# Optimization experiments

Measured on AMD Instinct MI355X. Metric: run time of the kernel, lower is better.

Reference implementation:

```python
import jax, jax.numpy as jnp
import numpy as np

N, D, H, E, K = 4096, 1024, 2048, 8, 2


def setup_inputs() -> dict:
    key = jax.random.key(0)
    ks = jax.random.split(key, 4)
    x = jax.random.normal(ks[0], (N, D), dtype=jnp.float32)
    w_gate = jax.random.normal(ks[1], (D, E), dtype=jnp.float32) * 0.02
    w1 = jax.random.normal(ks[2], (E, D, H), dtype=jnp.float32) * (1.0 / np.sqrt(D))
    b1 = jnp.zeros((E, H), dtype=jnp.float32)
    w2 = jax.random.normal(ks[3], (E, H, D), dtype=jnp.float32) * (1.0 / np.sqrt(H))
    b2 = jnp.zeros((E, D), dtype=jnp.float32)
    return {"x": x, "w_gate": w_gate, "w1": w1, "b1": b1, "w2": w2, "b2": b2}


def reference(x, w_gate, w1, b1, w2, b2):
    # --- top-k gating ---
    logits = x @ w_gate                      # [N, E]
    top_vals, top_idx = jax.lax.top_k(logits, K)   # [N, K]
    gates_k = jax.nn.softmax(top_vals, axis=-1)    # softmax over selected experts
    # scatter sparse gates into dense [N, E] combine weights (zeros off top-k)
    gates = jnp.zeros((x.shape[0], E), dtype=x.dtype)
    gates = gates.at[jnp.arange(x.shape[0])[:, None], top_idx].set(gates_k)
    # --- expert FFNs (computed densely over experts, combined sparsely) ---
    h = jax.nn.gelu(jnp.einsum('nd,edh->neh', x, w1) + b1[None])   # [N, E, H]
    y = jnp.einsum('neh,ehd->ned', h, w2) + b2[None]               # [N, E, D]
    out = jnp.einsum('ne,ned->nd', gates, y)                        # [N, D]
    return out
```

## Files before the change

kernel.cpp:

```cpp
#include <hip/hip_runtime.h>
#include <math.h>
#include <stdint.h>

#define N_TOK 4096
#define DIM   1024
#define HID   2048
#define NE    8
#define NROWS (N_TOK * 2)
#define LDST  72
#define OBST  128
#define TPT   16
#define CAP1  144
#define CAP2  72

typedef __attribute__((ext_vector_type(8))) short bf16x8;
typedef __attribute__((ext_vector_type(4))) float f32x4;

__device__ __forceinline__ unsigned short f2bf(float f) {
    union { unsigned int i; float f; } v; v.f = f;
    unsigned int u = v.i;
    return (unsigned short)((u + 0x7FFFu + ((u >> 16) & 1u)) >> 16);
}
__device__ __forceinline__ int clampi(int v, int lo, int hi) {
    return v < lo ? lo : (v > hi ? hi : v);
}
__device__ __forceinline__ void cvt8(const float* p, unsigned short* o) {
    float4 a = *(const float4*)p;
    float4 b = *(const float4*)(p + 4);
    o[0] = f2bf(a.x); o[1] = f2bf(a.y); o[2] = f2bf(a.z); o[3] = f2bf(a.w);
    o[4] = f2bf(b.x); o[5] = f2bf(b.y); o[6] = f2bf(b.z); o[7] = f2bf(b.w);
}
__device__ __forceinline__ float fast_gelu(float v) {
    float c = 0.7978845608028654f * (v + 0.044715f * v * v * v);
    float t = 1.f - 2.f / (1.f + __expf(2.f * c));
    return 0.5f * v * (1.f + t);
}
__device__ __forceinline__ void gload_lds16(const void* g, void* l) {
    __builtin_amdgcn_global_load_lds(
        (const __attribute__((address_space(1))) unsigned int*)g,
        (__attribute__((address_space(3))) unsigned int*)l,
        16, 0, 0);
}

__global__ __launch_bounds__(256) void gate_kernel(
    const float* __restrict__ x, const float* __restrict__ wg,
    unsigned short* __restrict__ top_e, float* __restrict__ top_g)
{
    int wave = threadIdx.x >> 6;
    int lane = threadIdx.x & 63;
    int n = blockIdx.x * 4 + wave;
    if (n >= N_TOK) return;
    float acc[NE];
#pragma unroll
    for (int e = 0; e < NE; e++) acc[e] = 0.f;
    const float* xrow = x + (size_t)n * DIM;
    for (int d = lane; d < DIM; d += 64) {
        float xv = xrow[d];
        float4 wa = *(const float4*)(wg + (size_t)d * NE);
        float4 wb = *(const float4*)(wg + (size_t)d * NE + 4);
        acc[0] += xv * wa.x; acc[1] += xv * wa.y;
        acc[2] += xv * wa.z; acc[3] += xv * wa.w;
        acc[4] += xv * wb.x; acc[5] += xv * wb.y;
        acc[6] += xv * wb.z; acc[7] += xv * wb.w;
    }
#pragma unroll
    for (int e = 0; e < NE; e++) {
        float v = acc[e];
#pragma unroll
        for (int off = 32; off > 0; off >>= 1) v += __shfl_xor(v, off, 64);
        acc[e] = v;
    }
    if (lane == 0) {
        int e0 = 0; float v0 = acc[0];
#pragma unroll
        for (int e = 1; e < NE; e++) if (acc[e] > v0) { v0 = acc[e]; e0 = e; }
        int e1 = (e0 == 0) ? 1 : 0; float v1 = acc[e1];
#pragma unroll
        for (int e = 0; e < NE; e++) if (e != e0 && acc[e] > v1) { v1 = acc[e]; e1 = e; }
        float s = expf(v1 - v0);
        float g0 = 1.f / (1.f + s);
        float g1 = s / (1.f + s);
        top_e[n] = (unsigned short)(e0 | (e1 << 8));
        top_g[2 * n + 0] = g0;
        top_g[2 * n + 1] = g1;
    }
}

__global__ __launch_bounds__(256) void scatter_plan_kernel(
    const unsigned short* __restrict__ top_e, const float* __restrict__ top_g,
    int* __restrict__ row_tok, float* __restrict__ row_gate,
    int* __restrict__ work1, int* __restrict__ work2)
{
    __shared__ int lpre[256][NE];
    __shared__ int etot[NE], ebase[NE];
    __shared__ int Tst[NE + 1];
    __shared__ int kept1[NE], ovb1[NE], fb1[NE + 1];
    __shared__ int kept2[NE], ovb2[NE], fb2[NE + 1];
    int t = threadIdx.x;

    unsigned long long c64 = 0ull;
    unsigned short te[TPT];
#pragma unroll
    for (int i = 0; i < TPT; i++) {
        int v = top_e[t * TPT + i];
        te[i] = (unsigned short)v;
        c64 += 1ull << ((v & 7) * 8);
        c64 += 1ull << (((v >> 8) & 7) * 8);
    }
#pragma unroll
    for (int e = 0; e < NE; e++) lpre[t][e] = (int)((c64 >> (e * 8)) & 0xFF);
    __syncthreads();

    if (t < NE) {
        int s = 0;
        for (int i = 0; i < 256; i++) { int c = lpre[i][t]; lpre[i][t] = s; s += c; }
        etot[t] = s;
    }
    __syncthreads();
    if (t == 0) {
        int b = 0, ts = 0;
#pragma unroll
        for (int e = 0; e < NE; e++) {
            ebase[e] = b; b += etot[e];
            Tst[e] = ts; ts += (etot[e] + 127) >> 7;
        }
        Tst[NE] = ts;
        int ob = 0, fs = 0;
#pragma unroll
        for (int e = 0; e < NE; e++) {
            int it = 16 * ((etot[e] + 127) >> 7);
            kept1[e] = (it < CAP1) ? it : CAP1;
            ovb1[e] = ob; ob += it - kept1[e];
            fb1[e] = fs; fs += CAP1 - kept1[e];
        }
        fb1[NE] = fs;
        ob = 0; fs = 0;
#pragma unroll
        for (int e = 0; e < NE; e++) {
            int it = 8 * ((etot[e] + 127) >> 7);
            kept2[e] = (it < CAP2) ? it : CAP2;
            ovb2[e] = ob; ob += it - kept2[e];
            fb2[e] = fs; fs += CAP2 - kept2[e];
        }
        fb2[NE] = fs;
    }
    __syncthreads();

    for (int i = t; i < NE * CAP1; i += 256) work1[i] = -1;
    for (int i = t; i < NE * CAP2; i += 256) work2[i] = -1;
    __syncthreads();

    int S = Tst[NE];
    for (int idx = t; idx < S * 16; idx += 256) {
        int s = idx >> 4, j = idx & 15;
        int e = 0;
#pragma unroll
        for (int k = 1; k < NE; k++) if (s >= Tst[k]) e = k;
        int sl = s - Tst[e];
        int gr0 = ebase[e] + sl * 128;
        int nv = etot[e] - sl * 128; if (nv > 128) nv = 128;
        int item = (gr0 << 16) | (nv << 8) | (e << 4) | j;
        int q = sl * 16 + j;
        int pos;
        if (q < kept1[e]) pos = e * CAP1 + q;
        else {
            int o = ovb1[e] + (q - kept1[e]);
            int xc = 0;
#pragma unroll
            for (int k = 1; k < NE; k++) if (o >= fb1[k]) xc = k;
            pos = xc * CAP1 + kept1[xc] + (o - fb1[xc]);
        }
        work1[clampi(pos, 0, NE * CAP1 - 1)] = item;
    }
    for (int idx = t; idx < S * 8; idx += 256) {
        int s = idx >> 3, j = idx & 7;
        int e = 0;
#pragma unroll
        for (int k = 1; k < NE; k++) if (s >= Tst[k]) e = k;
        int sl = s - Tst[e];
        int gr0 = ebase[e] + sl * 128;
        int nv = etot[e] - sl * 128; if (nv > 128) nv = 128;
        int item = (gr0 << 16) | (nv << 8) | (e << 4) | j;
        int q = sl * 8 + j;
        int pos;
        if (q < kept2[e]) pos = e * CAP2 + q;
        else {
            int o = ovb2[e] + (q - kept2[e]);
            int xc = 0;
#pragma unroll
            for (int k = 1; k < NE; k++) if (o >= fb2[k]) xc = k;
            pos = xc * CAP2 + kept2[xc] + (o - fb2[xc]);
        }
        work2[clampi(pos, 0, NE * CAP2 - 1)] = item;
    }

#pragma unroll
    for (int i = 0; i < TPT; i++) {
        int n = t * TPT + i;
        int v = te[i];
#pragma unroll
        for (int k = 0; k < 2; k++) {
            int e = (k ? (v >> 8) : v) & 7;
            int r = clampi(ebase[e] + lpre[t][e]++, 0, NROWS - 1);
            row_tok[r]  = (n << 1) | k;
            row_gate[r] = top_g[2 * n + k];
        }
    }
}

__global__ __launch_bounds__(256) void pack_x_kernel(
    const float* __restrict__ x, unsigned short* __restrict__ xb)
{
    size_t i = (size_t)(blockIdx.x * 256 + threadIdx.x) * 8;
    unsigned short o[8];
    cvt8(x + i, o);
    *(uint4*)(xb + i) = *(uint4*)o;
}

__global__ __launch_bounds__(256) void transpose_kernel(
    const float* __restrict__ in, unsigned short* __restrict__ outp, int K, int N)
{
    int e  = blockIdx.z;
    int kb = blockIdx.x;
    int nb = blockIdx.y;
    __shared__ __align__(16) unsigned short tile[64 * LDST];
    int t = threadIdx.x;

    int r = t >> 2, cq = t & 3;
    const float* sp = in + ((size_t)e * K + kb * 64 + r) * N + nb * 64 + cq * 16;
    unsigned short v[16];
    cvt8(sp, v);
    cvt8(sp + 8, v + 8);
    *(uint4*)(&tile[r * LDST + cq * 16 + 0]) = *(uint4*)(v + 0);
    *(uint4*)(&tile[r * LDST + cq * 16 + 8]) = *(uint4*)(v + 8);
    __syncthreads();

    int c = t >> 2, kq = t & 3;
    unsigned short o[16];
#pragma unroll
    for (int i = 0; i < 16; i++) o[i] = tile[(kq * 16 + i) * LDST + c];
    unsigned short* dp = outp + ((size_t)e * N + nb * 64 + c) * K + kb * 64 + kq * 16;
    *(uint4*)(dp + 0) = *(uint4*)(o + 0);
    *(uint4*)(dp + 8) = *(uint4*)(o + 8);
}

__global__ __launch_bounds__(256) void ffn1_fast6(
    const unsigned short* __restrict__ xb,
    const unsigned short* __restrict__ w1t,
    const float* __restrict__ b1,
    const int* __restrict__ work1,
    const int* __restrict__ row_tok,
    unsigned short* __restrict__ h)
{
    int lid = blockIdx.x;
    int wv = work1[(lid & 7) * CAP1 + (lid >> 3)];
    if (wv < 0) return;
    int nb     = wv & 15;
    int e      = (wv >> 4) & 7;
    int nvalid = (wv >> 8) & 0xFF;
    int gr0    = ((unsigned)wv) >> 16;

    __shared__ __align__(16) unsigned short lds[2 * 8192];
    __shared__ int ltok[128];

    int t = threadIdx.x;
    if (t < 128) {
        int rl = clampi(t, 0, nvalid - 1);
        int idx = clampi(gr0 + rl, 0, NROWS - 1);
        ltok[t] = clampi(row_tok[idx] >> 1, 0, N_TOK - 1);
    }
    __syncthreads();

    const int n0 = nb * 128;
    int w = t >> 6;
    const unsigned short* ga[4];
    const unsigned short* gb[4];
    int lofs[4];
#pragma unroll
    for (int i = 0; i < 4; i++) {
        int idx = i * 256 + t;
        int row = idx >> 3, cc = idx & 7;
        int ccs = cc ^ (row & 7);
        ga[i] = xb + (size_t)ltok[row] * DIM + ccs * 8;
        gb[i] = w1t + ((size_t)e * HID + n0 + row) * DIM + ccs * 8;
        lofs[i] = i * 2048 + w * 512;
    }

    int lane = t & 63, quad = lane >> 4, ln = lane & 15;
    int wr = w >> 1, wc = w & 1;
    int xr = ln & 7;
    f32x4 acc[4][4];
#pragma unroll
    for (int i = 0; i < 4; i++)
#pragma unroll
        for (int j = 0; j < 4; j++) acc[i][j] = (f32x4){0.f, 0.f, 0.f, 0.f};

    for (int kt = 0; kt < DIM / 64; kt++) {
        int k0 = kt * 64;
#pragma unroll
        for (int i = 0; i < 4; i++) {
            gload_lds16(ga[i] + k0, lds + lofs[i]);
            gload_lds16(gb[i] + k0, lds + 8192 + lofs[i]);
        }
        __syncthreads();
#pragma unroll
        for (int kk = 0; kk < 2; kk++) {
            bf16x8 af[4], bf[4];
#pragma unroll
            for (int s = 0; s < 4; s++)
                af[s] = *(const bf16x8*)(&lds[(wr * 64 + s * 16 + ln) * 64 + (((kk * 4 + quad) ^ xr) * 8)]);
#pragma unroll
            for (int s = 0; s < 4; s++)
                bf[s] = *(const bf16x8*)(&lds[8192 + (wc * 64 + s * 16 + ln) * 64 + (((kk * 4 + quad) ^ xr) * 8)]);
#pragma unroll
            for (int i = 0; i < 4; i++)
#pragma unroll
                for (int j = 0; j < 4; j++)
                    acc[i][j] = __builtin_amdgcn_mfma_f32_16x16x32_bf16(af[i], bf[j], acc[i][j], 0, 0, 0);
        }
        __syncthreads();
    }

    unsigned short* ob = lds;
#pragma unroll
    for (int j = 0; j < 4; j++) {
        int colL = wc * 64 + j * 16 + ln;
        float bias = b1[e * HID + n0 + colL];
#pragma unroll
        for (int i = 0; i < 4; i++) {
#pragma unroll
            for (int r = 0; r < 4; r++) {
                int m = wr * 64 + i * 16 + quad * 4 + r;
                ob[m * OBST + colL] = f2bf(fast_gelu(acc[i][j][r] + bias));
            }
        }
    }
    __syncthreads();
#pragma unroll
    for (int it = 0; it < 8; it++) {
        int idx = it * 256 + t;
        int m = idx >> 4, ch = idx & 15;
        if (m < nvalid)
            *(uint4*)(h + (size_t)(gr0 + m) * HID + n0 + ch * 8) = *(const uint4*)(ob + m * OBST + ch * 8);
    }
}

__global__ __launch_bounds__(256) void ffn2_fast8(
    const unsigned short* __restrict__ h,
    const unsigned short* __restrict__ w2t,
    const float* __restrict__ b2,
    const int* __restrict__ work2,
    const int* __restrict__ row_tok,
    const float* __restrict__ row_gate,
    float* __restrict__ out,
    float* __restrict__ ybuf1)
{
    int lid = blockIdx.x;
    int wv = work2[(lid & 7) * CAP2 + (lid >> 3)];
    if (wv < 0) return;
    int nb     = wv & 15;
    int e      = (wv >> 4) & 7;
    int nvalid = (wv >> 8) & 0xFF;
    int gr0    = ((unsigned)wv) >> 16;

    __shared__ __align__(16) unsigned short lds[2 * 8192];
    __shared__ int   ltok2[128];
    __shared__ float lgate[128];

    int t = threadIdx.x;
    if (t < 128) {
        int rl = clampi(t, 0, nvalid - 1);
        int idx = clampi(gr0 + rl, 0, NROWS - 1);
        ltok2[t] = clampi(row_tok[idx], 0, 2 * N_TOK - 1);
        lgate[t] = row_gate[idx];
    }
    __syncthreads();

    const int n0 = nb * 128;
    int w = t >> 6;
    const unsigned short* ga[4];
    const unsigned short* gb[4];
    int lofs[4];
#pragma unroll
    for (int i = 0; i < 4; i++) {
        int idx = i * 256 + t;
        int row = idx >> 3, cc = idx & 7;
        int ccs = cc ^ (row & 7);
        int arow = clampi(gr0 + row, 0, NROWS - 1);
        ga[i] = h + (size_t)arow * HID + ccs * 8;
        gb[i] = w2t + ((size_t)e * DIM + n0 + row) * HID + ccs * 8;
        lofs[i] = i * 2048 + w * 512;
    }

    int lane = t & 63, quad = lane >> 4, ln = lane & 15;
    int wr = w >> 1, wc = w & 1;
    int xr = ln & 7;
    f32x4 acc[4][4];
#pragma unroll
    for (int i = 0; i < 4; i++)
#pragma unroll
        for (int j = 0; j < 4; j++) acc[i][j] = (f32x4){0.f, 0.f, 0.f, 0.f};

    for (int kt = 0; kt < HID / 64; kt++) {
        int k0 = kt * 64;
#pragma unroll
        for (int i = 0; i < 4; i++) {
            gload_lds16(ga[i] + k0, lds + lofs[i]);
            gload_lds16(gb[i] + k0, lds + 8192 + lofs[i]);
        }
        __syncthreads();
#pragma unroll
        for (int kk = 0; kk < 2; kk++) {
            bf16x8 af[4], bf[4];
#pragma unroll
            for (int s = 0; s < 4; s++)
                af[s] = *(const bf16x8*)(&lds[(wr * 64 + s * 16 + ln) * 64 + (((kk * 4 + quad) ^ xr) * 8)]);
#pragma unroll
            for (int s = 0; s < 4; s++)
                bf[s] = *(const bf16x8*)(&lds[8192 + (wc * 64 + s * 16 + ln) * 64 + (((kk * 4 + quad) ^ xr) * 8)]);
#pragma unroll
            for (int i = 0; i < 4; i++)
#pragma unroll
                for (int j = 0; j < 4; j++)
                    acc[i][j] = __builtin_amdgcn_mfma_f32_16x16x32_bf16(af[i], bf[j], acc[i][j], 0, 0, 0);
        }
        __syncthreads();
    }

#pragma unroll
    for (int j = 0; j < 4; j++) {
        int col = n0 + wc * 64 + j * 16 + ln;
        float bias = b2[e * DIM + col];
#pragma unroll
        for (int i = 0; i < 4; i++) {
#pragma unroll
            for (int r = 0; r < 4; r++) {
                int m = wr * 64 + i * 16 + quad * 4 + r;
                if (m < nvalid) {
                    int rt  = ltok2[m];
                    int tok = rt >> 1;
                    float vv = (acc[i][j][r] + bias) * lgate[m];
                    float* dst = (rt & 1) ? ybuf1 : out;
                    dst[(size_t)tok * DIM + col] = vv;
                }
            }
        }
    }
}

__global__ __launch_bounds__(256) void combine_kernel(
    float4* __restrict__ out4, const float4* __restrict__ y4)
{
    int i = blockIdx.x * 256 + threadIdx.x;
    float4 a = out4[i];
    float4 b = y4[i];
    out4[i] = make_float4(a.x + b.x, a.y + b.y, a.z + b.z, a.w + b.w);
}

__global__ __launch_bounds__(256) void zero_out_kernel(float* __restrict__ out) {
    int i = blockIdx.x * 256 + threadIdx.x;
    out[i] = 0.f;
}

extern "C" void kernel_launch(void* const* d_in, const int* in_sizes, int n_in,
                              void* d_out, int out_size, void* d_ws, size_t ws_size,
                              hipStream_t stream) {
    const float* x  = (const float*)d_in[0];
    const float* wg = (const float*)d_in[1];
    const float* w1 = (const float*)d_in[2];
    const float* b1 = (const float*)d_in[3];
    const float* w2 = (const float*)d_in[4];
    const float* b2 = (const float*)d_in[5];
    float* out = (float*)d_out;

    char* ws = (char*)d_ws;
    unsigned short* top_e    = (unsigned short*)(ws + 256);
    float*          top_g    = (float*)(ws + 8448);
    int*            row_tok  = (int*)(ws + 41216);
    float*          row_gate = (float*)(ws + 73984);
    int*            work1    = (int*)(ws + 106752);
    int*            work2    = (int*)(ws + 111360);

    const size_t WT_OFF    = (size_t)1 << 17;
    const size_t HBUF_OFF  = WT_OFF + (size_t)NE * DIM * HID * 2;
    const size_t YBUF_OFF  = HBUF_OFF + (size_t)NROWS * HID * 2;
    const size_t NEEDED    = YBUF_OFF + (size_t)N_TOK * DIM * 4;

    if (ws_size < NEEDED) {
        zero_out_kernel<<<dim3(N_TOK * DIM / 256), dim3(256), 0, stream>>>(out);
        return;
    }

    unsigned short* wt    = (unsigned short*)(ws + WT_OFF);
    unsigned short* hbuf  = (unsigned short*)(ws + HBUF_OFF);
    float*          ybuf1 = (float*)(ws + YBUF_OFF);
    unsigned short* xb    = (unsigned short*)(ws + YBUF_OFF);

    gate_kernel<<<dim3(N_TOK / 4), dim3(256), 0, stream>>>(x, wg, top_e, top_g);
    scatter_plan_kernel<<<dim3(1), dim3(256), 0, stream>>>(top_e, top_g, row_tok, row_gate, work1, work2);
    pack_x_kernel<<<dim3(N_TOK * DIM / (256 * 8)), dim3(256), 0, stream>>>(x, xb);
    transpose_kernel<<<dim3(DIM / 64, HID / 64, NE), dim3(256), 0, stream>>>(w1, wt, DIM, HID);
    ffn1_fast6<<<dim3(NE * CAP1), dim3(256), 0, stream>>>(xb, wt, b1, work1, row_tok, hbuf);
    transpose_kernel<<<dim3(HID / 64, DIM / 64, NE), dim3(256), 0, stream>>>(w2, wt, HID, DIM);
    ffn2_fast8<<<dim3(NE * CAP2), dim3(256), 0, stream>>>(hbuf, wt, b2, work2, row_tok, row_gate, out, ybuf1);
    combine_kernel<<<dim3(N_TOK * DIM / 1024), dim3(256), 0, stream>>>((float4*)out, (const float4*)ybuf1);
}
```

Baseline: 374.7 us.

## Split FFN2 reduction dimension in two with atomic accumulation, reusing FFN1 work plan

The second expert GEMM now splits its hidden (K) dimension into two halves, doubling the number of work items so it reuses the ffn1 work list (16 items per 128-row slab). Partial results are accumulated with atomicAdd into out and ybuf1, which are zeroed by two new kernels beforehand; bias is added only by the first half. This aims to improve occupancy and load balance across CUs for the FFN2 phase, at the cost of atomic traffic, two extra zeroing passes and nondeterministic summation order.

New measurement: 420.2 us. 1.12x slower.

```diff
diff --git a/kernel.cpp b/kernel.cpp
--- a/kernel.cpp
+++ b/kernel.cpp
@@ -11,7 +11,6 @@
 #define OBST  128
 #define TPT   16
 #define CAP1  144
-#define CAP2  72
 
 typedef __attribute__((ext_vector_type(8))) short bf16x8;
 typedef __attribute__((ext_vector_type(4))) float f32x4;
@@ -89,13 +88,12 @@
 __global__ __launch_bounds__(256) void scatter_plan_kernel(
     const unsigned short* __restrict__ top_e, const float* __restrict__ top_g,
     int* __restrict__ row_tok, float* __restrict__ row_gate,
-    int* __restrict__ work1, int* __restrict__ work2)
+    int* __restrict__ work1)
 {
     __shared__ int lpre[256][NE];
     __shared__ int etot[NE], ebase[NE];
     __shared__ int Tst[NE + 1];
     __shared__ int kept1[NE], ovb1[NE], fb1[NE + 1];
-    __shared__ int kept2[NE], ovb2[NE], fb2[NE + 1];
     int t = threadIdx.x;
 
     unsigned long long c64 = 0ull;
@@ -134,20 +132,10 @@
             fb1[e] = fs; fs += CAP1 - kept1[e];
         }
         fb1[NE] = fs;
-        ob = 0; fs = 0;
-#pragma unroll
-        for (int e = 0; e < NE; e++) {
-            int it = 8 * ((etot[e] + 127) >> 7);
-            kept2[e] = (it < CAP2) ? it : CAP2;
-            ovb2[e] = ob; ob += it - kept2[e];
-            fb2[e] = fs; fs += CAP2 - kept2[e];
-        }
-        fb2[NE] = fs;
     }
     __syncthreads();
 
     for (int i = t; i < NE * CAP1; i += 256) work1[i] = -1;
-    for (int i = t; i < NE * CAP2; i += 256) work2[i] = -1;
     __syncthreads();
 
     int S = Tst[NE];
@@ -172,27 +160,6 @@
         }
         work1[clampi(pos, 0, NE * CAP1 - 1)] = item;
     }
-    for (int idx = t; idx < S * 8; idx += 256) {
-        int s = idx >> 3, j = idx & 7;
-        int e = 0;
-#pragma unroll
-        for (int k = 1; k < NE; k++) if (s >= Tst[k]) e = k;
-        int sl = s - Tst[e];
-        int gr0 = ebase[e] + sl * 128;
-        int nv = etot[e] - sl * 128; if (nv > 128) nv = 128;
-        int item = (gr0 << 16) | (nv << 8) | (e << 4) | j;
-        int q = sl * 8 + j;
-        int pos;
-        if (q < kept2[e]) pos = e * CAP2 + q;
-        else {
-            int o = ovb2[e] + (q - kept2[e]);
-            int xc = 0;
-#pragma unroll
-            for (int k = 1; k < NE; k++) if (o >= fb2[k]) xc = k;
-            pos = xc * CAP2 + kept2[xc] + (o - fb2[xc]);
-        }
-        work2[clampi(pos, 0, NE * CAP2 - 1)] = item;
-    }
 
 #pragma unroll
     for (int i = 0; i < TPT; i++) {
@@ -345,20 +312,22 @@
     }
 }
 
-__global__ __launch_bounds__(256) void ffn2_fast8(
+__global__ __launch_bounds__(256) void ffn2_fast9(
     const unsigned short* __restrict__ h,
     const unsigned short* __restrict__ w2t,
     const float* __restrict__ b2,
-    const int* __restrict__ work2,
+    const int* __restrict__ work1,
     const int* __restrict__ row_tok,
     const float* __restrict__ row_gate,
     float* __restrict__ out,
     float* __restrict__ ybuf1)
 {
     int lid = blockIdx.x;
-    int wv = work2[(lid & 7) * CAP2 + (lid >> 3)];
+    int wv = work1[(lid & 7) * CAP1 + (lid >> 3)];
     if (wv < 0) return;
-    int nb     = wv & 15;
+    int j4     = wv & 15;
+    int nb     = j4 & 7;
+    int kh     = j4 >> 3;
     int e      = (wv >> 4) & 7;
     int nvalid = (wv >> 8) & 0xFF;
     int gr0    = ((unsigned)wv) >> 16;
@@ -377,6 +346,7 @@
     __syncthreads();
 
     const int n0 = nb * 128;
+    const int kbase = kh * (HID / 2);
     int w = t >> 6;
     const unsigned short* ga[4];
     const unsigned short* gb[4];
@@ -387,8 +357,8 @@
         int row = idx >> 3, cc = idx & 7;
         int ccs = cc ^ (row & 7);
         int arow = clampi(gr0 + row, 0, NROWS - 1);
-        ga[i] = h + (size_t)arow * HID + ccs * 8;
-        gb[i] = w2t + ((size_t)e * DIM + n0 + row) * HID + ccs * 8;
+        ga[i] = h + (size_t)arow * HID + kbase + ccs * 8;
+        gb[i] = w2t + ((size_t)e * DIM + n0 + row) * HID + kbase + ccs * 8;
         lofs[i] = i * 2048 + w * 512;
     }
 
@@ -401,7 +371,7 @@
 #pragma unroll
         for (int j = 0; j < 4; j++) acc[i][j] = (f32x4){0.f, 0.f, 0.f, 0.f};
 
-    for (int kt = 0; kt < HID / 64; kt++) {
+    for (int kt = 0; kt < HID / 2 / 64; kt++) {
         int k0 = kt * 64;
 #pragma unroll
         for (int i = 0; i < 4; i++) {
@@ -430,7 +400,7 @@
 #pragma unroll
     for (int j = 0; j < 4; j++) {
         int col = n0 + wc * 64 + j * 16 + ln;
-        float bias = b2[e * DIM + col];
+        float bias = (kh == 0) ? b2[e * DIM + col] : 0.f;
 #pragma unroll
         for (int i = 0; i < 4; i++) {
 #pragma unroll
@@ -441,11 +411,15 @@
                     int tok = rt >> 1;
                     float vv = (acc[i][j][r] + bias) * lgate[m];
                     float* dst = (rt & 1) ? ybuf1 : out;
-                    dst[(size_t)tok * DIM + col] = vv;
+                    atomicAdd(&dst[(size_t)tok * DIM + col], vv);
                 }
             }
         }
     }
+}
+
+__global__ __launch_bounds__(256) void zero4_kernel(float4* __restrict__ p) {
+    p[blockIdx.x * 256 + threadIdx.x] = make_float4(0.f, 0.f, 0.f, 0.f);
 }
 
 __global__ __launch_bounds__(256) void combine_kernel(
@@ -479,7 +453,6 @@
     int*            row_tok  = (int*)(ws + 41216);
     float*          row_gate = (float*)(ws + 73984);
     int*            work1    = (int*)(ws + 106752);
-    int*            work2    = (int*)(ws + 111360);
 
     const size_t WT_OFF    = (size_t)1 << 17;
     const size_t HBUF_OFF  = WT_OFF + (size_t)NE * DIM * HID * 2;
@@ -497,11 +470,13 @@
     unsigned short* xb    = (unsigned short*)(ws + YBUF_OFF);
 
     gate_kernel<<<dim3(N_TOK / 4), dim3(256), 0, stream>>>(x, wg, top_e, top_g);
-    scatter_plan_kernel<<<dim3(1), dim3(256), 0, stream>>>(top_e, top_g, row_tok, row_gate, work1, work2);
+    scatter_plan_kernel<<<dim3(1), dim3(256), 0, stream>>>(top_e, top_g, row_tok, row_gate, work1);
     pack_x_kernel<<<dim3(N_TOK * DIM / (256 * 8)), dim3(256), 0, stream>>>(x, xb);
+    zero4_kernel<<<dim3(N_TOK * DIM / 1024), dim3(256), 0, stream>>>((float4*)out);
     transpose_kernel<<<dim3(DIM / 64, HID / 64, NE), dim3(256), 0, stream>>>(w1, wt, DIM, HID);
     ffn1_fast6<<<dim3(NE * CAP1), dim3(256), 0, stream>>>(xb, wt, b1, work1, row_tok, hbuf);
+    zero4_kernel<<<dim3(N_TOK * DIM / 1024), dim3(256), 0, stream>>>((float4*)ybuf1);
     transpose_kernel<<<dim3(HID / 64, DIM / 64, NE), dim3(256), 0, stream>>>(w2, wt, HID, DIM);
-    ffn2_fast8<<<dim3(NE * CAP2), dim3(256), 0, stream>>>(hbuf, wt, b2, work2, row_tok, row_gate, out, ybuf1);
+    ffn2_fast9<<<dim3(NE * CAP1), dim3(256), 0, stream>>>(hbuf, wt, b2, work1, row_tok, row_gate, out, ybuf1);
     combine_kernel<<<dim3(N_TOK * DIM / 1024), dim3(256), 0, stream>>>((float4*)out, (const float4*)ybuf1);
 }
```
